# Kernel optimization log

Hardware: AMD Instinct MI355X
Metric: run time of the kernel (lower is better)

## Reference

```python
import jax, jax.numpy as jnp
import numpy as np

H = 768
NH = 12
HD = H // NH
NDIM = 5
LN_EPS = 1e-5


def setup_inputs() -> dict:
    key = jax.random.key(0)
    ks = jax.random.split(key, 12)
    B, S = 4, 2048
    xavier = lambda k: jax.random.uniform(k, (H, H), jnp.float32, -1.0, 1.0) * np.sqrt(6.0 / (H + H))
    return {
        "hidden_states": jax.random.normal(ks[0], (B, S, H), jnp.float32),
        "Wq": xavier(ks[1]), "bq": jnp.zeros((H,), jnp.float32),
        "Wk": xavier(ks[2]), "bk": jnp.zeros((H,), jnp.float32),
        "Wv": xavier(ks[3]), "bv": jnp.zeros((H,), jnp.float32),
        "Wo": xavier(ks[4]), "bo": jnp.zeros((H,), jnp.float32),
        # per-dimension, per-head scalar biases (torch init: zeros; use small randn so grads are non-trivial)
        "dim_biases": 0.02 * jax.random.normal(ks[5], (NDIM, NH), jnp.float32),
        "ln_gamma": jnp.ones((H,), jnp.float32),
        "ln_beta": jnp.zeros((H,), jnp.float32),
        "attention_mask": jax.random.randint(ks[6], (4, 2048), 0, 2, jnp.int32),
        "dimension_idx": 2,
    }


def reference(hidden_states, Wq, bq, Wk, bk, Wv, bv, Wo, bo, dim_biases,
              ln_gamma, ln_beta, attention_mask, dimension_idx):
    B, S, _ = hidden_states.shape
    residual = hidden_states
    # torch nn.Linear: x @ W.T + b
    q = (hidden_states @ Wq.T + bq).reshape(B, S, NH, HD).transpose(0, 2, 1, 3)  # [B,NH,S,HD]
    k = (hidden_states @ Wk.T + bk).reshape(B, S, NH, HD).transpose(0, 2, 1, 3)
    v = (hidden_states @ Wv.T + bv).reshape(B, S, NH, HD).transpose(0, 2, 1, 3)

    scores = jnp.einsum("bhqd,bhkd->bhqk", q, k) / np.sqrt(HD)  # [B,NH,S,S]
    if dimension_idx is not None and dimension_idx < NDIM:
        scores = scores + dim_biases[dimension_idx][None, :, None, None]
    # mask over key positions, broadcast over heads and queries
    scores = jnp.where(attention_mask[:, None, None, :] == 0, -jnp.inf, scores)
    attn = jax.nn.softmax(scores, axis=-1)

    ctx = jnp.einsum("bhqk,bhkd->bhqd", attn, v)  # [B,NH,S,HD]
    ctx = ctx.transpose(0, 2, 1, 3).reshape(B, S, H)
    out = ctx @ Wo.T + bo

    y = out + residual
    mu = jnp.mean(y, axis=-1, keepdims=True)
    var = jnp.var(y, axis=-1, keepdims=True)
    y = (y - mu) / jnp.sqrt(var + LN_EPS) * ln_gamma + ln_beta
    return y
```

## Files before the change

kernel.cpp:

```cpp
#include <hip/hip_runtime.h>
#include <hip/hip_bf16.h>

#define HH    768
#define NHEAD 12
#define HDIM  64
#define BB    4
#define SS    2048
#define MM    (BB*SS)
#define NDIMS 5
#define WEL   (HH*HH)
#define LOG2E 1.44269504088896f
#define QSCALE 0.180336881f

typedef unsigned short u16;
typedef __attribute__((ext_vector_type(8))) short short8;
typedef __attribute__((ext_vector_type(4))) float floatx4;
typedef __attribute__((ext_vector_type(16))) float floatx16;

__device__ __forceinline__ float bf2f(u16 u) {
    return __uint_as_float(((unsigned int)u) << 16);
}
__device__ __forceinline__ u16 f2bf(float f) {
    unsigned int x = __float_as_uint(f);
    unsigned int r = (x + 0x7fffu + ((x >> 16) & 1u)) >> 16;
    return (u16)r;
}
__device__ __forceinline__ unsigned int pack_bf16x2(float a, float b) {
    float2 f2 = make_float2(a, b);
    __hip_bfloat162 h2 = __float22bfloat162_rn(f2);
    return *reinterpret_cast<unsigned int*>(&h2);
}
__device__ __forceinline__ void gld16(const u16* g, u16* l) {
    __builtin_amdgcn_global_load_lds(
        (const __attribute__((address_space(1))) unsigned int*)g,
        (__attribute__((address_space(3))) unsigned int*)l, 16, 0, 0);
}

__global__ __launch_bounds__(256) void f32_to_bf16(
    const float* __restrict__ in, u16* __restrict__ out, int n8)
{
    int i = blockIdx.x * 256 + threadIdx.x;
    if (i >= n8) return;
    float4 a = ((const float4*)in)[i*2];
    float4 b = ((const float4*)in)[i*2 + 1];
    ushort4 lo, hi;
    lo.x = f2bf(a.x); lo.y = f2bf(a.y); lo.z = f2bf(a.z); lo.w = f2bf(a.w);
    hi.x = f2bf(b.x); hi.y = f2bf(b.y); hi.z = f2bf(b.z); hi.w = f2bf(b.w);
    ((ushort4*)out)[i*2]     = lo;
    ((ushort4*)out)[i*2 + 1] = hi;
}

__global__ __launch_bounds__(256) void w_cvt4(
    const float* __restrict__ W0, const float* __restrict__ W1,
    const float* __restrict__ W2, const float* __restrict__ W3,
    u16* __restrict__ out)
{
    const float* src = (blockIdx.y == 0) ? W0 : (blockIdx.y == 1) ? W1
                     : (blockIdx.y == 2) ? W2 : W3;
    u16* dst = out + (size_t)blockIdx.y * WEL;
    int i = blockIdx.x * 256 + threadIdx.x;
    float4 a = ((const float4*)src)[i*2];
    float4 b = ((const float4*)src)[i*2 + 1];
    ushort4 lo, hi;
    lo.x = f2bf(a.x); lo.y = f2bf(a.y); lo.z = f2bf(a.z); lo.w = f2bf(a.w);
    hi.x = f2bf(b.x); hi.y = f2bf(b.y); hi.z = f2bf(b.z); hi.w = f2bf(b.w);
    ((ushort4*)dst)[i*2]     = lo;
    ((ushort4*)dst)[i*2 + 1] = hi;
}

__device__ __forceinline__ void gemm_gld_body(
    const u16* __restrict__ Xb, const u16* __restrict__ Wrows,
    const float* __restrict__ biasL, u16* __restrict__ outL, int i0)
{
    __shared__ u16 Xs[128][64];
    __shared__ u16 Ws[128][64];
    const int t = threadIdx.x;
    const int w = t >> 6, lane = t & 63;
    const int wy = w >> 1, wx = w & 1;
    const int m = lane & 31, hh = lane >> 5;

    const int grow = lane >> 3;
    const int cg   = (lane & 7) ^ grow;

    floatx16 acc[2][2];
    #pragma unroll
    for (int am = 0; am < 2; ++am)
        #pragma unroll
        for (int bn = 0; bn < 2; ++bn)
            #pragma unroll
            for (int r = 0; r < 16; ++r) acc[am][bn][r] = 0.f;

    for (int k0 = 0; k0 < HH; k0 += 64) {
        __syncthreads();
        #pragma unroll
        for (int j = 0; j < 4; ++j) {
            const int r = w*32 + j*8;
            gld16(Xb    + (size_t)(i0 + r + grow)*HH + k0 + cg*8, &Xs[r][0]);
            gld16(Wrows + (size_t)(r + grow)*HH      + k0 + cg*8, &Ws[r][0]);
        }
        __syncthreads();

        #pragma unroll
        for (int kh = 0; kh < 4; ++kh) {
            const int ch = kh*2 + hh;
            short8 af[2], bf[2];
            #pragma unroll
            for (int am = 0; am < 2; ++am) {
                const int row = wy*64 + am*32 + m;
                af[am] = *(const short8*)&Xs[row][(ch ^ (m & 7))*8];
            }
            #pragma unroll
            for (int bn = 0; bn < 2; ++bn) {
                const int row = wx*64 + bn*32 + m;
                bf[bn] = *(const short8*)&Ws[row][(ch ^ (m & 7))*8];
            }
            #pragma unroll
            for (int am = 0; am < 2; ++am)
                #pragma unroll
                for (int bn = 0; bn < 2; ++bn)
                    acc[am][bn] = __builtin_amdgcn_mfma_f32_32x32x16_bf16(
                        af[am], bf[bn], acc[am][bn], 0, 0, 0);
        }
    }

    float bb[2];
    #pragma unroll
    for (int bn = 0; bn < 2; ++bn) bb[bn] = biasL[wx*64 + bn*32 + m];
    #pragma unroll
    for (int am = 0; am < 2; ++am)
        #pragma unroll
        for (int bn = 0; bn < 2; ++bn)
            #pragma unroll
            for (int r = 0; r < 16; ++r) {
                int row = i0 + wy*64 + am*32 + (r & 3) + 8*(r >> 2) + 4*hh;
                outL[(size_t)row*HH + wx*64 + bn*32 + m] = f2bf(acc[am][bn][r] + bb[bn]);
            }
}

__global__ __launch_bounds__(256) void gemm_gld_qkv(
    const u16* __restrict__ Xb, const u16* __restrict__ Wb3,
    const float* __restrict__ bq, const float* __restrict__ bk, const float* __restrict__ bv,
    u16* __restrict__ oq, u16* __restrict__ ok, u16* __restrict__ ov)
{
    const int j0 = blockIdx.x * 128;
    const int sel = j0 / HH;
    const int lj = j0 - sel * HH;
    const float* bias = (sel == 0) ? bq : (sel == 1) ? bk : bv;
    u16* out = (sel == 0) ? oq : (sel == 1) ? ok : ov;
    gemm_gld_body(Xb, Wb3 + (size_t)j0 * HH, bias + lj, out + lj, blockIdx.y * 128);
}

__global__ __launch_bounds__(256) void gemm_gld_single(
    const u16* __restrict__ Xb, const u16* __restrict__ Wb,
    const float* __restrict__ bias, u16* __restrict__ out)
{
    const int j0 = blockIdx.x * 128;
    gemm_gld_body(Xb, Wb + (size_t)j0 * HH, bias + j0, out + j0, blockIdx.y * 128);
}

__global__ __launch_bounds__(256) void gemm_mfma_nt(
    const u16* __restrict__ Xb, const float* __restrict__ W,
    const float* __restrict__ bias, u16* __restrict__ out)
{
    __shared__ u16 Xs[128][40];
    __shared__ u16 Wt[64][40];
    const int t = threadIdx.x;
    const int w = t >> 6, lane = t & 63;
    const int c = lane & 15, qd = lane >> 4;
    const int i0 = blockIdx.y * 128, j0 = blockIdx.x * 64;
    const int xrow = t >> 1, xoff = (t & 1) * 16;
    const int wn = t >> 2, woff = (t & 3) * 8;

    floatx4 acc[2][4];
    #pragma unroll
    for (int mt = 0; mt < 2; ++mt)
        #pragma unroll
        for (int nt = 0; nt < 4; ++nt) acc[mt][nt] = (floatx4){0.f,0.f,0.f,0.f};

    for (int k0 = 0; k0 < HH; k0 += 32) {
        uint4 xa  = *(const uint4*)(Xb + (size_t)(i0 + xrow)*HH + k0 + xoff);
        uint4 xb2 = *(const uint4*)(Xb + (size_t)(i0 + xrow)*HH + k0 + xoff + 8);
        float4 wa = *(const float4*)(W + (size_t)(j0 + wn)*HH + k0 + woff);
        float4 wb = *(const float4*)(W + (size_t)(j0 + wn)*HH + k0 + woff + 4);
        __syncthreads();
        *(uint4*)&Xs[xrow][xoff]     = xa;
        *(uint4*)&Xs[xrow][xoff + 8] = xb2;
        ushort4 w0, w1;
        w0.x = f2bf(wa.x); w0.y = f2bf(wa.y); w0.z = f2bf(wa.z); w0.w = f2bf(wa.w);
        w1.x = f2bf(wb.x); w1.y = f2bf(wb.y); w1.z = f2bf(wb.z); w1.w = f2bf(wb.w);
        *(ushort4*)&Wt[wn][woff]     = w0;
        *(ushort4*)&Wt[wn][woff + 4] = w1;
        __syncthreads();

        short8 a0 = *(const short8*)&Xs[w*32 + c][qd*8];
        short8 a1 = *(const short8*)&Xs[w*32 + 16 + c][qd*8];
        #pragma unroll
        for (int nt = 0; nt < 4; ++nt) {
            short8 bfr = *(const short8*)&Wt[nt*16 + c][qd*8];
            acc[0][nt] = __builtin_amdgcn_mfma_f32_16x16x32_bf16(a0, bfr, acc[0][nt], 0, 0, 0);
            acc[1][nt] = __builtin_amdgcn_mfma_f32_16x16x32_bf16(a1, bfr, acc[1][nt], 0, 0, 0);
        }
    }

    float bv[4];
    #pragma unroll
    for (int nt = 0; nt < 4; ++nt) bv[nt] = bias[j0 + nt*16 + c];
    #pragma unroll
    for (int mt = 0; mt < 2; ++mt)
        #pragma unroll
        for (int nt = 0; nt < 4; ++nt)
            #pragma unroll
            for (int r = 0; r < 4; ++r)
                out[(size_t)(i0 + w*32 + mt*16 + qd*4 + r)*HH + j0 + nt*16 + c] =
                    f2bf(acc[mt][nt][r] + bv[nt]);
}

__global__ __launch_bounds__(256, 3) void attn_mfma(
    const u16* __restrict__ Q, const u16* __restrict__ K, const u16* __restrict__ V,
    const float* __restrict__ dim_biases, const int* __restrict__ mask,
    const int* __restrict__ dim_idx_p, u16* __restrict__ ctx)
{
    __shared__ u16 Ks[64][72];
    __shared__ unsigned int Vt2[64][36];
    __shared__ u16 Pt[4][2][16][72];
    __shared__ float madd[64];

    const int t = threadIdx.x;
    const int w = t >> 6, lane = t & 63;
    const int c = lane & 15, qd = lane >> 4;
    const int b = blockIdx.z, h = blockIdx.y;
    const int q0 = blockIdx.x * 128;

    const int didx = *dim_idx_p;
    const float db2 = ((didx < NDIMS) ? dim_biases[didx*NHEAD + h] : 0.f) * LOG2E;

    short8 ones;
    #pragma unroll
    for (int j = 0; j < 8; ++j) ones[j] = (short)0x3F80;

    short8 qf[2][2];
    #pragma unroll
    for (int g = 0; g < 2; ++g) {
        const u16* qsrc = Q + ((size_t)(b*SS + q0 + w*32 + g*16 + c))*HH + h*HDIM;
        #pragma unroll
        for (int kc = 0; kc < 2; ++kc) {
            ushort4 u0 = *(const ushort4*)(qsrc + kc*32 + qd*8);
            ushort4 u1 = *(const ushort4*)(qsrc + kc*32 + qd*8 + 4);
            const u16 uu[8] = {u0.x,u0.y,u0.z,u0.w,u1.x,u1.y,u1.z,u1.w};
            #pragma unroll
            for (int j = 0; j < 8; ++j)
                qf[g][kc][j] = (short)f2bf(bf2f(uu[j]) * QSCALE);
        }
    }

    floatx4 o[2][4], lacc[2];
    #pragma unroll
    for (int g = 0; g < 2; ++g) {
        lacc[g] = (floatx4){0.f,0.f,0.f,0.f};
        #pragma unroll
        for (int dt = 0; dt < 4; ++dt) o[g][dt] = (floatx4){0.f,0.f,0.f,0.f};
    }

    const int skey = t >> 2, sdp = (t & 3) * 16;
    const int vkp = t & 31, vdg = (t >> 5) * 8;

    for (int kt = 0; kt < SS/64; ++kt) {
        __syncthreads();
        {
            const u16* ksrc = K + ((size_t)(b*SS + kt*64 + skey))*HH + h*HDIM + sdp;
            *(uint4*)&Ks[skey][sdp]     = *(const uint4*)ksrc;
            *(uint4*)&Ks[skey][sdp + 8] = *(const uint4*)(ksrc + 8);
            const u16* va = V + ((size_t)(b*SS + kt*64 + 2*vkp))*HH + h*HDIM + vdg;
            const u16* vb = va + HH;
            ushort4 a0 = *(const ushort4*)va;
            ushort4 a1 = *(const ushort4*)(va + 4);
            ushort4 b0 = *(const ushort4*)vb;
            ushort4 b1 = *(const ushort4*)(vb + 4);
            const u16 aa[8] = {a0.x,a0.y,a0.z,a0.w,a1.x,a1.y,a1.z,a1.w};
            const u16 bb[8] = {b0.x,b0.y,b0.z,b0.w,b1.x,b1.y,b1.z,b1.w};
            #pragma unroll
            for (int i = 0; i < 8; ++i)
                Vt2[vdg + i][vkp] = (unsigned int)aa[i] | ((unsigned int)bb[i] << 16);
            if (t < 64)
                madd[t] = (mask[(size_t)b*SS + kt*64 + t] != 0) ? db2 : -1e30f;
        }
        __syncthreads();

        floatx4 z[2][4];
        {
            short8 ka[4][2];
            #pragma unroll
            for (int mt = 0; mt < 4; ++mt) {
                ka[mt][0] = *(const short8*)&Ks[mt*16 + c][qd*8];
                ka[mt][1] = *(const short8*)&Ks[mt*16 + c][32 + qd*8];
            }
            #pragma unroll
            for (int g = 0; g < 2; ++g)
                #pragma unroll
                for (int mt = 0; mt < 4; ++mt) {
                    floatx4 zz = __builtin_amdgcn_mfma_f32_16x16x32_bf16(ka[mt][0], qf[g][0], (floatx4){0.f,0.f,0.f,0.f}, 0, 0, 0);
                    z[g][mt] = __builtin_amdgcn_mfma_f32_16x16x32_bf16(ka[mt][1], qf[g][1], zz, 0, 0, 0);
                }
        }

        #pragma unroll
        for (int g = 0; g < 2; ++g) {
            #pragma unroll
            for (int mt = 0; mt < 4; ++mt) {
                unsigned int pk[2];
                #pragma unroll
                for (int half = 0; half < 2; ++half) {
                    float p0 = __builtin_amdgcn_exp2f(z[g][mt][half*2]     + madd[mt*16 + qd*4 + half*2]);
                    float p1 = __builtin_amdgcn_exp2f(z[g][mt][half*2 + 1] + madd[mt*16 + qd*4 + half*2 + 1]);
                    pk[half] = pack_bf16x2(p0, p1);
                }
                *(uint2*)&Pt[w][g][c][mt*16 + qd*4] = make_uint2(pk[0], pk[1]);
            }
        }

        {
            short8 vt[2][4];
            #pragma unroll
            for (int kc = 0; kc < 2; ++kc)
                #pragma unroll
                for (int dt = 0; dt < 4; ++dt)
                    vt[kc][dt] = *(const short8*)&Vt2[dt*16 + c][kc*16 + qd*4];
            #pragma unroll
            for (int g = 0; g < 2; ++g)
                #pragma unroll
                for (int kc = 0; kc < 2; ++kc) {
                    short8 ap = *(const short8*)&Pt[w][g][c][kc*32 + qd*8];
                    lacc[g] = __builtin_amdgcn_mfma_f32_16x16x32_bf16(ap, ones, lacc[g], 0, 0, 0);
                    #pragma unroll
                    for (int dt = 0; dt < 4; ++dt)
                        o[g][dt] = __builtin_amdgcn_mfma_f32_16x16x32_bf16(ap, vt[kc][dt], o[g][dt], 0, 0, 0);
                }
        }
    }

    #pragma unroll
    for (int g = 0; g < 2; ++g) {
        #pragma unroll
        for (int r = 0; r < 4; ++r) {
            float lr = lacc[g][r];
            float inv = (lr > 0.f) ? 1.f / lr : 0.f;
            u16* dst = ctx + ((size_t)(b*SS + q0 + w*32 + g*16 + qd*4 + r))*HH + h*HDIM + c;
            #pragma unroll
            for (int dt = 0; dt < 4; ++dt)
                dst[dt*16] = f2bf(o[g][dt][r] * inv);
        }
    }
}

__global__ __launch_bounds__(256) void add_ln_wave(
    const u16* __restrict__ proj, const float* __restrict__ resid,
    const float* __restrict__ gamma, const float* __restrict__ beta,
    float* __restrict__ out)
{
    const int t = threadIdx.x, w = t >> 6, lane = t & 63;
    const int row = blockIdx.x * 4 + w;
    const size_t base = (size_t)row * HH + lane * 12;
    const int gbase = lane * 12;

    float x[12];
    #pragma unroll
    for (int j = 0; j < 3; ++j) {
        ushort4 p = *(const ushort4*)(proj + base + j*4);
        float4  r = *(const float4*)(resid + base + j*4);
        x[j*4+0] = bf2f(p.x) + r.x;
        x[j*4+1] = bf2f(p.y) + r.y;
        x[j*4+2] = bf2f(p.z) + r.z;
        x[j*4+3] = bf2f(p.w) + r.w;
    }
    float s = 0.f, ss = 0.f;
    #pragma unroll
    for (int j = 0; j < 12; ++j) { s += x[j]; ss += x[j]*x[j]; }
    #pragma unroll
    for (int off = 1; off < 64; off <<= 1) {
        s  += __shfl_xor(s, off);
        ss += __shfl_xor(ss, off);
    }
    float mean = s * (1.f/768.f);
    float var  = ss * (1.f/768.f) - mean*mean;
    float rstd = rsqrtf(fmaxf(var, 0.f) + 1e-5f);
    #pragma unroll
    for (int j = 0; j < 3; ++j) {
        float4 g = *(const float4*)(gamma + gbase + j*4);
        float4 bt = *(const float4*)(beta + gbase + j*4);
        float4 y;
        y.x = (x[j*4+0]-mean)*rstd*g.x + bt.x;
        y.y = (x[j*4+1]-mean)*rstd*g.y + bt.y;
        y.z = (x[j*4+2]-mean)*rstd*g.z + bt.z;
        y.w = (x[j*4+3]-mean)*rstd*g.w + bt.w;
        *(float4*)(out + base + j*4) = y;
    }
}

extern "C" void kernel_launch(void* const* d_in, const int* in_sizes, int n_in,
                              void* d_out, int out_size, void* d_ws, size_t ws_size,
                              hipStream_t stream)
{
    (void)in_sizes; (void)n_in; (void)out_size;
    const float* x    = (const float*)d_in[0];
    const float* Wq   = (const float*)d_in[1];
    const float* bq   = (const float*)d_in[2];
    const float* Wk   = (const float*)d_in[3];
    const float* bk   = (const float*)d_in[4];
    const float* Wv   = (const float*)d_in[5];
    const float* bv   = (const float*)d_in[6];
    const float* Wo   = (const float*)d_in[7];
    const float* bo   = (const float*)d_in[8];
    const float* dimb = (const float*)d_in[9];
    const float* gam  = (const float*)d_in[10];
    const float* bet  = (const float*)d_in[11];
    const int* mask   = (const int*)d_in[12];
    const int* didx   = (const int*)d_in[13];

    const size_t N = (size_t)MM * HH;
    if (ws_size < 4 * N * sizeof(u16)) return;
    u16* ws = (u16*)d_ws;
    u16* q    = ws;
    u16* kbuf = ws + N;
    u16* vbuf = ws + 2*N;
    u16* slot3 = ws + 3*N;
    u16* xb   = slot3;
    u16* ctx  = slot3;
    u16* proj = q;

    const bool bigws = ws_size >= (4 * N + 4 * (size_t)WEL) * sizeof(u16);
    u16* wb = ws + 4 * N;

    f32_to_bf16<<<(int)(N/8/256), 256, 0, stream>>>(x, xb, (int)(N/8));
    if (bigws) {
        w_cvt4<<<dim3(WEL/8/256, 4), 256, 0, stream>>>(Wq, Wk, Wv, Wo, wb);
        gemm_gld_qkv<<<dim3(3*HH/128, MM/128), 256, 0, stream>>>(
            xb, wb, bq, bk, bv, q, kbuf, vbuf);
    } else {
        dim3 gg(HH/64, MM/128);
        gemm_mfma_nt<<<gg, 256, 0, stream>>>(xb, Wq, bq, q);
        gemm_mfma_nt<<<gg, 256, 0, stream>>>(xb, Wk, bk, kbuf);
        gemm_mfma_nt<<<gg, 256, 0, stream>>>(xb, Wv, bv, vbuf);
    }
    attn_mfma<<<dim3(SS/128, NHEAD, BB), 256, 0, stream>>>(q, kbuf, vbuf, dimb, mask, didx, ctx);
    if (bigws) gemm_gld_single<<<dim3(HH/128, MM/128), 256, 0, stream>>>(ctx, wb + 3*WEL, bo, proj);
    else {
        dim3 gg(HH/64, MM/128);
        gemm_mfma_nt<<<gg, 256, 0, stream>>>(ctx, Wo, bo, proj);
    }
    add_ln_wave<<<MM/4, 256, 0, stream>>>(proj, x, gam, bet, (float*)d_out);
}
```

Baseline: 266.2 us.

## Rewrite attention with 32x32 MFMA, register-resident P, and double-buffered K/V

```diff
diff --git a/kernel.cpp b/kernel.cpp
--- a/kernel.cpp
+++ b/kernel.cpp
@@ -16,6 +16,8 @@
 typedef __attribute__((ext_vector_type(8))) short short8;
 typedef __attribute__((ext_vector_type(4))) float floatx4;
 typedef __attribute__((ext_vector_type(16))) float floatx16;
+typedef __attribute__((ext_vector_type(4))) unsigned int uint4v;
+typedef __attribute__((ext_vector_type(2))) unsigned int uint2v;
 
 __device__ __forceinline__ float bf2f(u16 u) {
     return __uint_as_float(((unsigned int)u) << 16);
@@ -215,140 +217,139 @@
                     f2bf(acc[mt][nt][r] + bv[nt]);
 }
 
-__global__ __launch_bounds__(256, 3) void attn_mfma(
+__global__ __launch_bounds__(256, 3) void attn_mfma32(
     const u16* __restrict__ Q, const u16* __restrict__ K, const u16* __restrict__ V,
     const float* __restrict__ dim_biases, const int* __restrict__ mask,
     const int* __restrict__ dim_idx_p, u16* __restrict__ ctx)
 {
-    __shared__ u16 Ks[64][72];
-    __shared__ unsigned int Vt2[64][36];
-    __shared__ u16 Pt[4][2][16][72];
-    __shared__ float madd[64];
+    __shared__ u16 Ks[2][64][64];
+    __shared__ u16 Vt[2][64][64];
+    __shared__ float madd[2][64];
 
     const int t = threadIdx.x;
     const int w = t >> 6, lane = t & 63;
-    const int c = lane & 15, qd = lane >> 4;
-    const int b = blockIdx.z, h = blockIdx.y;
-    const int q0 = blockIdx.x * 128;
+    const int ql = lane & 31, hi = lane >> 5;
+    const int sw7 = ql & 7;
+
+    const int flat = blockIdx.x + 16 * (blockIdx.y + 12 * blockIdx.z);
+    const int swz  = (flat & 7) * 96 + (flat >> 3);
+    const int q0 = (swz & 15) * 128;
+    const int h  = (swz >> 4) % NHEAD;
+    const int b  = swz / (16 * NHEAD);
 
     const int didx = *dim_idx_p;
     const float db2 = ((didx < NDIMS) ? dim_biases[didx*NHEAD + h] : 0.f) * LOG2E;
 
+    const int grow = lane >> 3;
+    const int cg   = (lane & 7) ^ grow;
+    const int vkp = t & 31;
+    const int vdg = (t >> 5) * 8;
+
     short8 ones;
     #pragma unroll
     for (int j = 0; j < 8; ++j) ones[j] = (short)0x3F80;
 
-    short8 qf[2][2];
-    #pragma unroll
-    for (int g = 0; g < 2; ++g) {
-        const u16* qsrc = Q + ((size_t)(b*SS + q0 + w*32 + g*16 + c))*HH + h*HDIM;
-        #pragma unroll
-        for (int kc = 0; kc < 2; ++kc) {
-            ushort4 u0 = *(const ushort4*)(qsrc + kc*32 + qd*8);
-            ushort4 u1 = *(const ushort4*)(qsrc + kc*32 + qd*8 + 4);
+    short8 qv[4];
+    {
+        const u16* qsrc = Q + ((size_t)(b*SS + q0 + w*32 + ql))*HH + h*HDIM + 8*hi;
+        #pragma unroll
+        for (int s = 0; s < 4; ++s) {
+            ushort4 u0 = *(const ushort4*)(qsrc + s*16);
+            ushort4 u1 = *(const ushort4*)(qsrc + s*16 + 4);
             const u16 uu[8] = {u0.x,u0.y,u0.z,u0.w,u1.x,u1.y,u1.z,u1.w};
             #pragma unroll
             for (int j = 0; j < 8; ++j)
-                qf[g][kc][j] = (short)f2bf(bf2f(uu[j]) * QSCALE);
-        }
-    }
-
-    floatx4 o[2][4], lacc[2];
-    #pragma unroll
-    for (int g = 0; g < 2; ++g) {
-        lacc[g] = (floatx4){0.f,0.f,0.f,0.f};
-        #pragma unroll
-        for (int dt = 0; dt < 4; ++dt) o[g][dt] = (floatx4){0.f,0.f,0.f,0.f};
-    }
-
-    const int skey = t >> 2, sdp = (t & 3) * 16;
-    const int vkp = t & 31, vdg = (t >> 5) * 8;
+                qv[s][j] = (short)f2bf(bf2f(uu[j]) * QSCALE);
+        }
+    }
+
+    floatx16 o[2], lacc;
+    #pragma unroll
+    for (int r = 0; r < 16; ++r) { o[0][r] = 0.f; o[1][r] = 0.f; lacc[r] = 0.f; }
+
+    auto stage = [&](int kt, int buf) {
+        #pragma unroll
+        for (int j = 0; j < 2; ++j) {
+            const int rbase = w*16 + j*8;
+            gld16(K + (size_t)(b*SS + kt*64 + rbase + grow)*HH + h*HDIM + cg*8,
+                  &Ks[buf][rbase][0]);
+        }
+        const u16* va = V + ((size_t)(b*SS + kt*64 + 2*vkp))*HH + h*HDIM + vdg;
+        const u16* vb = va + HH;
+        ushort4 a0 = *(const ushort4*)va;
+        ushort4 a1 = *(const ushort4*)(va + 4);
+        ushort4 b0 = *(const ushort4*)vb;
+        ushort4 b1 = *(const ushort4*)(vb + 4);
+        const u16 aa[8] = {a0.x,a0.y,a0.z,a0.w,a1.x,a1.y,a1.z,a1.w};
+        const u16 bb[8] = {b0.x,b0.y,b0.z,b0.w,b1.x,b1.y,b1.z,b1.w};
+        #pragma unroll
+        for (int i = 0; i < 8; ++i) {
+            const int d = vdg + i;
+            const int sc = (vkp >> 2) ^ (d & 7);
+            *(unsigned int*)&Vt[buf][d][sc*8 + (vkp & 3)*2] =
+                (unsigned int)aa[i] | ((unsigned int)bb[i] << 16);
+        }
+        if (t < 64)
+            madd[buf][t] = (mask[(size_t)b*SS + kt*64 + t] != 0) ? db2 : -1e30f;
+    };
+
+    stage(0, 0);
 
     for (int kt = 0; kt < SS/64; ++kt) {
+        const int cur = kt & 1;
         __syncthreads();
-        {
-            const u16* ksrc = K + ((size_t)(b*SS + kt*64 + skey))*HH + h*HDIM + sdp;
-            *(uint4*)&Ks[skey][sdp]     = *(const uint4*)ksrc;
-            *(uint4*)&Ks[skey][sdp + 8] = *(const uint4*)(ksrc + 8);
-            const u16* va = V + ((size_t)(b*SS + kt*64 + 2*vkp))*HH + h*HDIM + vdg;
-            const u16* vb = va + HH;
-            ushort4 a0 = *(const ushort4*)va;
-            ushort4 a1 = *(const ushort4*)(va + 4);
-            ushort4 b0 = *(const ushort4*)vb;
-            ushort4 b1 = *(const ushort4*)(vb + 4);
-            const u16 aa[8] = {a0.x,a0.y,a0.z,a0.w,a1.x,a1.y,a1.z,a1.w};
-            const u16 bb[8] = {b0.x,b0.y,b0.z,b0.w,b1.x,b1.y,b1.z,b1.w};
-            #pragma unroll
-            for (int i = 0; i < 8; ++i)
-                Vt2[vdg + i][vkp] = (unsigned int)aa[i] | ((unsigned int)bb[i] << 16);
-            if (t < 64)
-                madd[t] = (mask[(size_t)b*SS + kt*64 + t] != 0) ? db2 : -1e30f;
-        }
-        __syncthreads();
-
-        floatx4 z[2][4];
-        {
-            short8 ka[4][2];
-            #pragma unroll
-            for (int mt = 0; mt < 4; ++mt) {
-                ka[mt][0] = *(const short8*)&Ks[mt*16 + c][qd*8];
-                ka[mt][1] = *(const short8*)&Ks[mt*16 + c][32 + qd*8];
-            }
-            #pragma unroll
-            for (int g = 0; g < 2; ++g)
+        if (kt + 1 < SS/64) stage(kt + 1, cur ^ 1);
+
+        #pragma unroll
+        for (int kblk = 0; kblk < 2; ++kblk) {
+            const int krow = kblk*32 + ql;
+            const u16* kb = &Ks[cur][krow][0];
+
+            floatx16 z;
+            #pragma unroll
+            for (int qq = 0; qq < 4; ++qq) {
+                float4 mv = *(const float4*)&madd[cur][kblk*32 + qq*8 + 4*hi];
+                z[qq*4+0] = mv.x; z[qq*4+1] = mv.y; z[qq*4+2] = mv.z; z[qq*4+3] = mv.w;
+            }
+            #pragma unroll
+            for (int s = 0; s < 4; ++s) {
+                short8 kf = *(const short8*)(kb + ((s*2 + hi) ^ sw7)*8);
+                z = __builtin_amdgcn_mfma_f32_32x32x16_bf16(kf, qv[s], z, 0, 0, 0);
+            }
+            #pragma unroll
+            for (int r = 0; r < 16; ++r) z[r] = __builtin_amdgcn_exp2f(z[r]);
+
+            #pragma unroll
+            for (int ks = 0; ks < 2; ++ks) {
+                unsigned x0 = pack_bf16x2(z[ks*8 + 0], z[ks*8 + 1]);
+                unsigned y0 = pack_bf16x2(z[ks*8 + 4], z[ks*8 + 5]);
+                unsigned x1 = pack_bf16x2(z[ks*8 + 2], z[ks*8 + 3]);
+                unsigned y1 = pack_bf16x2(z[ks*8 + 6], z[ks*8 + 7]);
+                uint2v s0 = __builtin_amdgcn_permlane32_swap(x0, y0, false, false);
+                uint2v s1 = __builtin_amdgcn_permlane32_swap(x1, y1, false, false);
+                uint4v pv; pv[0] = s0[0]; pv[1] = s1[0]; pv[2] = s0[1]; pv[3] = s1[1];
+                short8 pa = __builtin_bit_cast(short8, pv);
+
+                lacc = __builtin_amdgcn_mfma_f32_32x32x16_bf16(pa, ones, lacc, 0, 0, 0);
+                const int ck = kblk*4 + ks*2 + hi;
                 #pragma unroll
-                for (int mt = 0; mt < 4; ++mt) {
-                    floatx4 zz = __builtin_amdgcn_mfma_f32_16x16x32_bf16(ka[mt][0], qf[g][0], (floatx4){0.f,0.f,0.f,0.f}, 0, 0, 0);
-                    z[g][mt] = __builtin_amdgcn_mfma_f32_16x16x32_bf16(ka[mt][1], qf[g][1], zz, 0, 0, 0);
+                for (int dblk = 0; dblk < 2; ++dblk) {
+                    const int d = dblk*32 + ql;
+                    short8 vf = *(const short8*)&Vt[cur][d][(ck ^ sw7)*8];
+                    o[dblk] = __builtin_amdgcn_mfma_f32_32x32x16_bf16(pa, vf, o[dblk], 0, 0, 0);
                 }
-        }
-
-        #pragma unroll
-        for (int g = 0; g < 2; ++g) {
-            #pragma unroll
-            for (int mt = 0; mt < 4; ++mt) {
-                unsigned int pk[2];
-                #pragma unroll
-                for (int half = 0; half < 2; ++half) {
-                    float p0 = __builtin_amdgcn_exp2f(z[g][mt][half*2]     + madd[mt*16 + qd*4 + half*2]);
-                    float p1 = __builtin_amdgcn_exp2f(z[g][mt][half*2 + 1] + madd[mt*16 + qd*4 + half*2 + 1]);
-                    pk[half] = pack_bf16x2(p0, p1);
-                }
-                *(uint2*)&Pt[w][g][c][mt*16 + qd*4] = make_uint2(pk[0], pk[1]);
-            }
-        }
-
-        {
-            short8 vt[2][4];
-            #pragma unroll
-            for (int kc = 0; kc < 2; ++kc)
-                #pragma unroll
-                for (int dt = 0; dt < 4; ++dt)
-                    vt[kc][dt] = *(const short8*)&Vt2[dt*16 + c][kc*16 + qd*4];
-            #pragma unroll
-            for (int g = 0; g < 2; ++g)
-                #pragma unroll
-                for (int kc = 0; kc < 2; ++kc) {
-                    short8 ap = *(const short8*)&Pt[w][g][c][kc*32 + qd*8];
-                    lacc[g] = __builtin_amdgcn_mfma_f32_16x16x32_bf16(ap, ones, lacc[g], 0, 0, 0);
-                    #pragma unroll
-                    for (int dt = 0; dt < 4; ++dt)
-                        o[g][dt] = __builtin_amdgcn_mfma_f32_16x16x32_bf16(ap, vt[kc][dt], o[g][dt], 0, 0, 0);
-                }
-        }
-    }
-
-    #pragma unroll
-    for (int g = 0; g < 2; ++g) {
-        #pragma unroll
-        for (int r = 0; r < 4; ++r) {
-            float lr = lacc[g][r];
-            float inv = (lr > 0.f) ? 1.f / lr : 0.f;
-            u16* dst = ctx + ((size_t)(b*SS + q0 + w*32 + g*16 + qd*4 + r))*HH + h*HDIM + c;
-            #pragma unroll
-            for (int dt = 0; dt < 4; ++dt)
-                dst[dt*16] = f2bf(o[g][dt][r] * inv);
-        }
+            }
+        }
+    }
+
+    #pragma unroll
+    for (int r = 0; r < 16; ++r) {
+        float l = lacc[r];
+        float inv = (l > 0.f) ? 1.f / l : 0.f;
+        const int qrow = q0 + w*32 + (r & 3) + 8*(r >> 2) + 4*hi;
+        u16* dst = ctx + ((size_t)(b*SS + qrow))*HH + h*HDIM + ql;
+        dst[0]  = f2bf(o[0][r] * inv);
+        dst[32] = f2bf(o[1][r] * inv);
     }
 }
 
@@ -441,7 +442,7 @@
         gemm_mfma_nt<<<gg, 256, 0, stream>>>(xb, Wk, bk, kbuf);
         gemm_mfma_nt<<<gg, 256, 0, stream>>>(xb, Wv, bv, vbuf);
     }
-    attn_mfma<<<dim3(SS/128, NHEAD, BB), 256, 0, stream>>>(q, kbuf, vbuf, dimb, mask, didx, ctx);
+    attn_mfma32<<<dim3(SS/128, NHEAD, BB), 256, 0, stream>>>(q, kbuf, vbuf, dimb, mask, didx, ctx);
     if (bigws) gemm_gld_single<<<dim3(HH/128, MM/128), 256, 0, stream>>>(ctx, wb + 3*WEL, bo, proj);
     else {
         dim3 gg(HH/64, MM/128);
```

Result: faster. 260.1 us (-2.3%).
